# Optimization experiments

Measured on AMD Instinct MI355X. Metric: run time of the kernel, lower is better.

Reference implementation:

```python
import jax, jax.numpy as jnp
import numpy as np

PAD, BOS = 0, 1
EPS = 1e-08


def _lstm_cell(xt, h, c, wih, whh, bih, bhh):
    z = xt @ wih.T + h @ whh.T + bih + bhh
    i, f, g, o = jnp.split(z, 4, axis=-1)  # torch gate order i,f,g,o
    c = jax.nn.sigmoid(f) * c + jax.nn.sigmoid(i) * jnp.tanh(g)
    h = jax.nn.sigmoid(o) * jnp.tanh(c)
    return h, c


def _run_lstm(emb, wih, whh, bih, bhh):
    B, H = emb.shape[0], whh.shape[1]
    def step(carry, xt):
        h, c = _lstm_cell(xt, carry[0], carry[1], wih, whh, bih, bhh)
        return (h, c), h
    init = (jnp.zeros((B, H), emb.dtype), jnp.zeros((B, H), emb.dtype))
    (hT, cT), outs = jax.lax.scan(step, init, jnp.swapaxes(emb, 0, 1))
    return jnp.swapaxes(outs, 0, 1), hT, cT


def setup_inputs() -> dict:
    key = jax.random.key(0)
    V, H, B, S, T = 32000, 256, 8, 200, 51
    ks = jax.random.split(key, 24)
    def n(i, shape, s=0.02):
        return jax.random.normal(ks[i], shape, jnp.float32) * s
    x = jax.random.randint(ks[0], (B, S), 1, V)
    x = x.at[:, -1].set(V - 1)  # pins extended vocab size to 2V
    labels = jax.random.randint(ks[1], (B, T), 1, V)
    return {
        "x": x, "labels": labels, "ext_vocab_size": 2 * V,
        "emb_enc": n(2, (V, H)).at[PAD].set(0.0),
        "wih_f": n(3, (4 * H, H)), "whh_f": n(4, (4 * H, H)),
        "bih_f": jnp.zeros((4 * H,), jnp.float32), "bhh_f": jnp.zeros((4 * H,), jnp.float32),
        "wih_b": n(5, (4 * H, H)), "whh_b": n(6, (4 * H, H)),
        "bih_b": jnp.zeros((4 * H,), jnp.float32), "bhh_b": jnp.zeros((4 * H,), jnp.float32),
        "w_sel1": n(7, (H, 2 * H)), "b_sel1": jnp.zeros((H,), jnp.float32),
        "w_sel2": n(8, (1, H)), "b_sel2": jnp.zeros((1,), jnp.float32),
        "w_rh": n(9, (H, 2 * H)), "b_rh": jnp.zeros((H,), jnp.float32),
        "w_rc": n(10, (H, 2 * H)), "b_rc": jnp.zeros((H,), jnp.float32),
        "emb_dec": n(11, (V, H)).at[PAD].set(0.0),
        "wih_d": n(12, (4 * H, 3 * H)), "whh_d": n(13, (4 * H, H)),
        "bih_d": jnp.zeros((4 * H,), jnp.float32), "bhh_d": jnp.zeros((4 * H,), jnp.float32),
        "w_attn": n(14, (H, 4 * H)), "b_attn": jnp.zeros((H,), jnp.float32),
        "w_attn_v": n(15, (1, H)),
        "w_ptr": n(16, (1, 3 * H)), "b_ptr": jnp.zeros((1,), jnp.float32),
        "w_gen": n(17, (V, H)), "b_gen": jnp.zeros((V,), jnp.float32),
        "w_cov": n(18, (H, 1)), "b_cov": jnp.zeros((H,), jnp.float32),
    }


def reference(x, labels, ext_vocab_size, emb_enc, wih_f, whh_f, bih_f, bhh_f,
              wih_b, whh_b, bih_b, bhh_b, w_sel1, b_sel1, w_sel2, b_sel2,
              w_rh, b_rh, w_rc, b_rc, emb_dec, wih_d, whh_d, bih_d, bhh_d,
              w_attn, b_attn, w_attn_v, w_ptr, b_ptr, w_gen, b_gen, w_cov, b_cov):
    B, S = x.shape
    V, H = w_gen.shape
    # ---- Encoder: BiLSTM (no padding -> packing is identity; eval -> no dropout)
    emb = emb_enc[x]  # [B,S,H]
    out_f, h_f, c_f = _run_lstm(emb, wih_f, whh_f, bih_f, bhh_f)
    out_b_r, h_b, c_b = _run_lstm(emb[:, ::-1], wih_b, whh_b, bih_b, bhh_b)
    enc_out = jnp.concatenate([out_f, out_b_r[:, ::-1]], axis=-1)  # [B,S,2H]
    copy_probs = jax.nn.sigmoid(
        (jnp.tanh(enc_out @ w_sel1.T + b_sel1) @ w_sel2.T + b_sel2)[..., 0])  # [B,S]
    # ---- bidirectional state reduction
    h0 = jax.nn.relu(jnp.concatenate([h_f, h_b], -1) @ w_rh.T + b_rh)
    c0 = jax.nn.relu(jnp.concatenate([c_f, c_b], -1) @ w_rc.T + b_rc)
    # ---- Decoder loop (teacher forcing): inputs = [BOS, labels[:,1:T-1]]
    dec_in = jnp.concatenate(
        [jnp.full((B, 1), BOS, labels.dtype), labels[:, 1:-1]], axis=1)  # [B,T-1]
    mask_cp = (copy_probs > EPS).astype(jnp.float32)
    rows = jnp.arange(B)[:, None]

    def step(carry, tok):
        h, c, cov = carry
        cov_feat = cov[..., None] * w_cov[:, 0] + b_cov  # [B,S,H]
        feats = jnp.concatenate(
            [enc_out, jnp.broadcast_to(h[:, None, :], (B, S, H)), cov_feat], axis=-1)
        e = jnp.tanh(feats @ w_attn.T + b_attn)           # [B,S,H]
        attn = jax.nn.softmax(e @ w_attn_v[0], axis=1)    # [B,S]
        attn = attn * mask_cp
        attn = attn / (attn.sum(1, keepdims=True) + 1e-10)
        cov = cov + attn
        ctx = jnp.einsum('bs,bsd->bd', attn, enc_out)     # [B,2H]
        h, c = _lstm_cell(jnp.concatenate([emb_dec[tok], ctx], -1), h, c,
                          wih_d, whh_d, bih_d, bhh_d)
        p_gen = jax.nn.sigmoid(jnp.concatenate([ctx, h], -1) @ w_ptr.T + b_ptr)  # [B,1]
        vocab_dist = jax.nn.softmax(h @ w_gen.T + b_gen, axis=-1)  # [B,V]
        dist = jnp.zeros((B, ext_vocab_size), jnp.float32)
        dist = dist.at[:, :V].set(p_gen * vocab_dist)
        dist = dist.at[rows, x].add((1.0 - p_gen) * attn)  # pointer/copy scatter-add
        return (h, c, cov), dist

    cov0 = jnp.zeros((B, S), jnp.float32)
    _, outs = jax.lax.scan(step, (h0, c0, cov0), dec_in.T)
    outputs = jnp.swapaxes(outs, 0, 1)  # [B,T-1,EV]
    # ---- loss (faithful: CE treats the mixture distribution as logits)
    targets = labels[:, 1:]
    logp = jax.nn.log_softmax(outputs, axis=-1)
    nll = -jnp.take_along_axis(logp, targets[..., None], axis=-1)[..., 0]
    valid = (targets != PAD).astype(jnp.float32)
    loss_ce = (nll * valid).sum() / valid.sum()
    m = (x != PAD).astype(jnp.float32)
    lp = jnp.clip(jnp.log(copy_probs), -100.0, None)
    l1p = jnp.clip(jnp.log1p(-copy_probs), -100.0, None)
    bce = -(m * lp + (1.0 - m) * l1p)
    loss = loss_ce + 1.0 * (bce * m).sum() / m.sum()
    return outputs, loss
```

## Files before the change

### kernel.cpp

```cpp
#include <hip/hip_runtime.h>
#include <hip/hip_bf16.h>
#include <stdint.h>


#define DEVI __device__ __forceinline__
#define AT_RLX __ATOMIC_RELAXED
#define SC_AGT __HIP_MEMORY_SCOPE_AGENT

static constexpr size_t OFF_ACC   = 0;
static constexpr size_t OFF_FLAGE = 4;
static constexpr size_t OFF_FLAGD = 36;
static constexpr size_t ZERO_FLOATS = 200;
static constexpr size_t OFF_CTX   = 256;
static constexpr size_t OFF_EMB   = 4352;
static constexpr size_t OFF_HSEL  = OFF_EMB;
static constexpr size_t OFF_HP    = OFF_EMB;
static constexpr size_t OFF_DHP   = OFF_EMB;
static constexpr size_t OFF_DPE   = OFF_EMB + 8192;
static constexpr size_t OFF_DCX   = OFF_EMB + 20992;
static constexpr size_t DTAG_FLOATS = 53760;
static constexpr size_t OFF_PREF  = OFF_EMB  + 409600;
static constexpr size_t OFF_PREB  = OFF_PREF + 1638400;
static constexpr size_t OFF_BIAS  = OFF_PREB + 1638400;
static constexpr size_t OFF_HB    = OFF_BIAS + 3072;
static constexpr size_t OFF_HFIN  = OFF_HB   + 8192;
static constexpr size_t OFF_CFIN  = OFF_HFIN + 4096;
static constexpr size_t OFF_ENCOUT= OFF_CFIN + 4096;
static constexpr size_t OFF_MASK  = OFF_ENCOUT + 819200;
static constexpr size_t OFF_C0    = OFF_MASK + 1600;
static constexpr size_t OFF_EP    = OFF_C0   + 2048;
static constexpr size_t OFF_WCP   = OFF_EP   + 409600;
static constexpr size_t OFF_BCP   = OFF_WCP  + 256;
static constexpr size_t OFF_DEMB  = OFF_BCP  + 256;
static constexpr size_t OFF_DPRE  = OFF_DEMB + 102400;
static constexpr size_t OFF_HBUF  = OFF_DPRE + 409600;
static constexpr size_t OFF_CS    = OFF_HBUF + 4096;
static constexpr size_t OFF_HS    = OFF_CS   + 204800;
static constexpr size_t OFF_AS    = OFF_HS   + 102400;
static constexpr size_t OFF_PG    = OFF_AS   + 80000;
static constexpr size_t OFF_PE    = OFF_PG   + 512;

DEVI float sigf(float x)      { return 1.0f / (1.0f + __expf(-x)); }
DEVI float tanh_fast(float x) { return 1.0f - 2.0f / (1.0f + __expf(2.0f * x)); }
DEVI float ald(const float* p)  { return __hip_atomic_load((float*)p, AT_RLX, SC_AGT); }
DEVI void  ast(float* p, float v){ __hip_atomic_store(p, v, AT_RLX, SC_AGT); }
DEVI unsigned long long aldu(const unsigned long long* p) {
  return __hip_atomic_load((unsigned long long*)p, AT_RLX, SC_AGT);
}
DEVI void astu(unsigned long long* p, unsigned long long v) {
  __hip_atomic_store(p, v, AT_RLX, SC_AGT);
}

__global__ __launch_bounds__(256) void k_biassum(
    const float* bih_f, const float* bhh_f, const float* bih_b, const float* bhh_b,
    const float* bih_d, const float* bhh_d, float* ws) {
  int i = blockIdx.x * 256 + threadIdx.x;
  int which = i >> 10, jj = i & 1023;
  float v = (which == 0) ? bih_f[jj] + bhh_f[jj]
          : (which == 1) ? bih_b[jj] + bhh_b[jj]
                         : bih_d[jj] + bhh_d[jj];
  ws[OFF_BIAS + i] = v;
}

__global__ __launch_bounds__(256) void k_embed(
    const int* xin, const int* labels, const float* emb_enc, const float* emb_dec, float* ws) {
  int r = blockIdx.x, h = threadIdx.x;
  if (r < 1600) {
    int t = r >> 3, b = r & 7;
    ws[OFF_EMB + (size_t)r * 256 + h] = emb_enc[(size_t)xin[b * 200 + t] * 256 + h];
  } else {
    int r2 = r - 1600;
    int t = r2 >> 3, b = r2 & 7;
    int tok = (t == 0) ? 1 : labels[b * 51 + t];
    ws[OFF_DEMB + (size_t)r2 * 256 + h] = emb_dec[(size_t)tok * 256 + h];
  }
}

template<int BM, int BN, int TM, int TN, int CMAP, int ACT, int AMAP>
__global__ __launch_bounds__(256) void k_gemm(
    const float* __restrict__ A, const float* __restrict__ B,
    const float* __restrict__ bias, float* __restrict__ C,
    int M, int K, int ldb, int ldc) {
  __shared__ float As[16][BM];
  __shared__ float Bs[16][BN];
  const int tid = threadIdx.x;
  const int tx = tid & 15, ty = tid >> 4;
  const int m0 = blockIdx.x * BM, n0 = blockIdx.y * BN;
  float acc[TM][TN];
#pragma unroll
  for (int i = 0; i < TM; ++i)
#pragma unroll
    for (int q = 0; q < TN; ++q) acc[i][q] = 0.f;

  for (int kk = 0; kk < K; kk += 16) {
#pragma unroll
    for (int e = tid; e < BM * 4; e += 256) {
      int m = e >> 2, k4 = (e & 3) * 4;
      int gm0 = m0 + m;
      float4 v = {0.f, 0.f, 0.f, 0.f};
      if (gm0 < M) {
        int gm = AMAP ? (((199 - (gm0 >> 3)) << 3) + (gm0 & 7)) : gm0;
        v = *(const float4*)(A + (size_t)gm * K + kk + k4);
      }
      As[k4 + 0][m] = v.x; As[k4 + 1][m] = v.y; As[k4 + 2][m] = v.z; As[k4 + 3][m] = v.w;
    }
#pragma unroll
    for (int e = tid; e < BN * 4; e += 256) {
      int n = e >> 2, k4 = (e & 3) * 4;
      float4 v = *(const float4*)(B + (size_t)(n0 + n) * ldb + kk + k4);
      Bs[k4 + 0][n] = v.x; Bs[k4 + 1][n] = v.y; Bs[k4 + 2][n] = v.z; Bs[k4 + 3][n] = v.w;
    }
    __syncthreads();
#pragma unroll
    for (int k = 0; k < 16; ++k) {
      float a[TM], bv[TN];
#pragma unroll
      for (int i = 0; i < TM; ++i) a[i] = As[k][ty * TM + i];
#pragma unroll
      for (int q = 0; q < TN; ++q) bv[q] = Bs[k][tx * TN + q];
#pragma unroll
      for (int i = 0; i < TM; ++i)
#pragma unroll
        for (int q = 0; q < TN; ++q) acc[i][q] += a[i] * bv[q];
    }
    __syncthreads();
  }
#pragma unroll
  for (int i = 0; i < TM; ++i) {
    int gm = m0 + ty * TM + i;
    if (gm >= M) continue;
    size_t base;
    if (CMAP == 1) { int t = gm >> 3, b = gm & 7; base = (size_t)(b * 50 + t) * 64000; }
    else            base = (size_t)gm * ldc;
#pragma unroll
    for (int q = 0; q < TN; ++q) {
      int n = n0 + tx * TN + q;
      float v = acc[i][q] + bias[n];
      if (ACT == 1) v = tanh_fast(v);
      C[base + n] = v;
    }
  }
}

__global__ __launch_bounds__(512, 1) void k_encoder(
    const float* __restrict__ whh_f, const float* __restrict__ whh_b, float* __restrict__ ws) {
  __shared__ float hs2[2048];
  __shared__ float zs[512];
  const int dir = blockIdx.x >> 4;
  const int p   = blockIdx.x & 15;
  const int u0  = p * 16;
  const float* whh = dir ? whh_b : whh_f;
  const float* pre = ws + (dir ? OFF_PREB : OFF_PREF);
  unsigned long long* hp = (unsigned long long*)(ws + OFF_HP);
  const int tid = threadIdx.x;
  const int kc4 = tid & 15;
  const int jp  = tid >> 4;
  const int jj0 = jp * 2, jj1 = jj0 + 1;
  const int jg0 = (jj0 >> 4) * 256 + u0 + (jj0 & 15);
  const int jg1 = (jj1 >> 4) * 256 + u0 + (jj1 & 15);
  float4 W0[4], W1[4];
  {
    const float* w0 = whh + (size_t)jg0 * 256 + kc4 * 16;
    const float* w1 = whh + (size_t)jg1 * 256 + kc4 * 16;
#pragma unroll
    for (int q = 0; q < 4; ++q) { W0[q] = *(const float4*)(w0 + q * 4);
                                  W1[q] = *(const float4*)(w1 + q * 4); }
  }
  const int jlf = kc4 >> 3, bf = kc4 & 7;
  const int jjf = jp * 2 + jlf;
  const int jf  = (jjf >> 4) * 256 + u0 + (jjf & 15);
  const int zsl = (jjf >> 4) * 128 + (jjf & 15) * 8 + bf;
  const int wb_ = tid >> 6;
  const int kk0 = (tid * 4) & 255;
  const int wdst = wb_ * 256 + ((kk0 >> 2) & 3) * 64 + (kk0 >> 4) * 4;
  const int ui2 = tid & 15, b2 = tid >> 4;
  float c_reg = 0.f;
  float* enc = ws + OFF_ENCOUT;

  for (int t = 0; t < 200; ++t) {
    float pre_v = pre[((size_t)t * 8 + bf) * 1024 + jf];
    float acc[16];
#pragma unroll
    for (int i = 0; i < 16; ++i) acc[i] = 0.f;
    if (t > 0) {
      unsigned long long* src = hp + (size_t)((((t + 1) & 1) * 2 + dir) * 2048) + tid * 4;
      const unsigned long long e = (unsigned long long)(unsigned)t;
      unsigned long long a0, a1, a2, a3;
      for (;;) {
        a0 = aldu(src + 0); a1 = aldu(src + 1); a2 = aldu(src + 2); a3 = aldu(src + 3);
        if (((a0 >> 32) == e) && ((a1 >> 32) == e) &&
            ((a2 >> 32) == e) && ((a3 >> 32) == e)) break;
        __builtin_amdgcn_s_sleep(1);
      }
      float4 hv;
      hv.x = __uint_as_float((unsigned)a0);
      hv.y = __uint_as_float((unsigned)a1);
      hv.z = __uint_as_float((unsigned)a2);
      hv.w = __uint_as_float((unsigned)a3);
      *(float4*)(&hs2[wdst]) = hv;
    }
    __syncthreads();
    if (t > 0) {
#pragma unroll
      for (int b = 0; b < 8; ++b) {
        const float* hb = &hs2[b * 256 + kc4 * 4];
#pragma unroll
        for (int q = 0; q < 4; ++q) {
          float4 h4 = *(const float4*)(hb + q * 64);
          acc[b]     = fmaf(W0[q].x, h4.x, acc[b]);
          acc[b]     = fmaf(W0[q].y, h4.y, acc[b]);
          acc[b]     = fmaf(W0[q].z, h4.z, acc[b]);
          acc[b]     = fmaf(W0[q].w, h4.w, acc[b]);
          acc[8 + b] = fmaf(W1[q].x, h4.x, acc[8 + b]);
          acc[8 + b] = fmaf(W1[q].y, h4.y, acc[8 + b]);
          acc[8 + b] = fmaf(W1[q].z, h4.z, acc[8 + b]);
          acc[8 + b] = fmaf(W1[q].w, h4.w, acc[8 + b]);
        }
      }
    }
    {
      bool h8 = (kc4 & 8) != 0;
#pragma unroll
      for (int i = 0; i < 8; ++i) {
        float send = h8 ? acc[i] : acc[i + 8];
        float keep = h8 ? acc[i + 8] : acc[i];
        acc[i] = keep + __shfl_xor(send, 8);
      }
      bool h4b = (kc4 & 4) != 0;
#pragma unroll
      for (int i = 0; i < 4; ++i) {
        float send = h4b ? acc[i] : acc[i + 4];
        float keep = h4b ? acc[i + 4] : acc[i];
        acc[i] = keep + __shfl_xor(send, 4);
      }
      bool h2b = (kc4 & 2) != 0;
#pragma unroll
      for (int i = 0; i < 2; ++i) {
        float send = h2b ? acc[i] : acc[i + 2];
        float keep = h2b ? acc[i + 2] : acc[i];
        acc[i] = keep + __shfl_xor(send, 2);
      }
      bool h1b = (kc4 & 1) != 0;
      {
        float send = h1b ? acc[0] : acc[1];
        float keep = h1b ? acc[1] : acc[0];
        acc[0] = keep + __shfl_xor(send, 1);
      }
    }
    zs[zsl] = acc[0] + pre_v;
    __syncthreads();
    if (tid < 128) {
      int i0 = ui2 * 8 + b2;
      float zi = zs[i0], zf = zs[128 + i0], zg = zs[256 + i0], zo = zs[384 + i0];
      float cn = sigf(zf) * c_reg + sigf(zi) * tanh_fast(zg);
      float hn = sigf(zo) * tanh_fast(cn);
      c_reg = cn;
      int uu = u0 + ui2;
      if (t < 199) {
        unsigned long long pk =
            ((unsigned long long)(unsigned)(t + 1) << 32) |
            (unsigned long long)__float_as_uint(hn);
        astu(hp + (size_t)(((t & 1) * 2 + dir) * 2048) + b2 * 256 + uu, pk);
      }
      int s = dir ? (199 - t) : t;
      enc[((size_t)b2 * 200 + s) * 512 + dir * 256 + uu] = hn;
      if (t == 199) {
        ws[OFF_HFIN + (size_t)(dir * 8 + b2) * 256 + uu] = hn;
        ws[OFF_CFIN + (size_t)(dir * 8 + b2) * 256 + uu] = cn;
      }
    }
  }
}

__global__ __launch_bounds__(64) void k_selbce(
    const float* w_sel2, const float* b_sel2, const int* xin, float* ws) {
  int r = blockIdx.x, lane = threadIdx.x;
  float pacc = 0.f;
#pragma unroll
  for (int i = 0; i < 4; ++i) {
    int k = lane + 64 * i;
    pacc += ws[OFF_HSEL + (size_t)r * 256 + k] * w_sel2[k];
  }
#pragma unroll
  for (int m = 1; m < 64; m <<= 1) pacc += __shfl_xor(pacc, m);
  if (lane == 0) {
    float cp = sigf(pacc + b_sel2[0]);
    ws[OFF_MASK + r] = (cp > 1e-8f) ? 1.f : 0.f;
    int b = r / 200, s = r % 200;
    float m = (xin[b * 200 + s] != 0) ? 1.f : 0.f;
    if (m > 0.f) {
      float lp = fmaxf(logf(cp), -100.f);
      atomicAdd(ws + OFF_ACC + 2, -lp);
    }
    atomicAdd(ws + OFF_ACC + 3, m);
  }
}

__global__ __launch_bounds__(256) void k_wcp(
    const float* w_attn, const float* w_cov, const float* b_cov, float* ws) {
  int jj = threadIdx.x;
  float a = 0.f, c = 0.f;
  for (int h = 0; h < 256; ++h) {
    float w = w_attn[(size_t)jj * 1024 + 768 + h];
    a += w * w_cov[h];
    c += w * b_cov[h];
  }
  ws[OFF_WCP + jj] = a;
  ws[OFF_BCP + jj] = c;
}

__global__ __launch_bounds__(256) void k_h0c0(
    const float* w_rh, const float* b_rh, const float* w_rc, const float* b_rc, float* ws) {
  int b = blockIdx.x, jj = threadIdx.x;
  const float* hf  = ws + OFF_HFIN + (size_t)b * 256;
  const float* hbk = ws + OFF_HFIN + 2048 + (size_t)b * 256;
  const float* cf  = ws + OFF_CFIN + (size_t)b * 256;
  const float* cbk = ws + OFF_CFIN + 2048 + (size_t)b * 256;
  float ah = b_rh[jj], ac = b_rc[jj];
  for (int k = 0; k < 256; ++k) {
    ah += hf[k] * w_rh[(size_t)jj * 512 + k];
    ac += cf[k] * w_rc[(size_t)jj * 512 + k];
  }
  for (int k = 0; k < 256; ++k) {
    ah += hbk[k] * w_rh[(size_t)jj * 512 + 256 + k];
    ac += cbk[k] * w_rc[(size_t)jj * 512 + 256 + k];
  }
  ws[OFF_C0 + (size_t)b * 256 + jj] = fmaxf(ac, 0.f);
  unsigned long long* hp2 = (unsigned long long*)(ws + OFF_DHP);
  hp2[(size_t)b * 256 + jj] = (unsigned long long)__float_as_uint(fmaxf(ah, 0.f));
}

__global__ __launch_bounds__(512, 1) void k_decoder(
    const float* __restrict__ wih_d, const float* __restrict__ whh_d,
    const float* __restrict__ w_attn, const float* __restrict__ w_attn_v,
    float* __restrict__ ws) {
  __shared__ float hc_s[8 * 768];
  __shared__ float h_pad[264];
  __shared__ float hw_q[64];
  __shared__ float e_s[256];
  __shared__ float at_s[256], cv_s[256], msk_s[256];
  __shared__ float zs_l[256];
  __shared__ float wcq_s[64], bcq_s[64], wvq_s[64];
  __shared__ float mS_s[2];
  const int g = blockIdx.x, tid = threadIdx.x;
  const int b1 = g >> 2, sq = g & 3, s0 = sq * 50;
  unsigned long long* hp2 = (unsigned long long*)(ws + OFF_DHP);
  unsigned long long* pe2 = (unsigned long long*)(ws + OFF_DPE);
  unsigned long long* cx2 = (unsigned long long*)(ws + OFF_DCX);
  const int jl = tid >> 3, kq = tid & 7;
  const int kseg = tid & 15, row_l = tid >> 4;
  const int u_l = row_l & 7, gate = row_l >> 3;
  const int j = gate * 256 + g * 8 + u_l;
  float4 W48[12];
#pragma unroll
  for (int q = 0; q < 12; ++q) {
    int k0 = 4 * kseg + 64 * q;
    W48[q] = (k0 < 512) ? *(const float4*)(wih_d + (size_t)j * 768 + 256 + k0)
                        : *(const float4*)(whh_d + (size_t)j * 256 + (k0 - 512));
  }
  float4 W32[8];
  {
    const float* wsrc = w_attn + (size_t)(sq * 64 + jl) * 1024 + 512 + kq * 32;
#pragma unroll
    for (int q = 0; q < 8; ++q) W32[q] = *(const float4*)(wsrc + q * 4);
  }
  const int u_c = tid & 7, b_c = tid >> 3;
  float c_reg = (tid < 64) ? ws[OFF_C0 + (size_t)b_c * 256 + g * 8 + u_c] : 0.f;
  for (int s = tid; s < 256; s += 512) {
    msk_s[s] = (s < 200) ? ws[OFF_MASK + b1 * 200 + s] : 0.f;
    cv_s[s] = 0.f;
  }
  if (tid < 64) {
    wcq_s[tid] = ws[OFF_WCP + sq * 64 + tid];
    bcq_s[tid] = ws[OFF_BCP + sq * 64 + tid];
    wvq_s[tid] = w_attn_v[sq * 64 + tid];
  }
  __syncthreads();

  for (int t = 0; t < 50; ++t) {
    const int rb = t & 1, wb = 1 - rb;
    const unsigned long long tgH = (unsigned long long)(unsigned)t;
    const unsigned long long tgP = (unsigned long long)(unsigned)(t + 1);
    if (tid < 256) {
      unsigned long long* src = hp2 + (size_t)rb * 2048 + b1 * 256 + tid;
      unsigned long long v;
      for (;;) {
        v = aldu(src);
        if ((v >> 32) == tgH) break;
        __builtin_amdgcn_s_sleep(1);
      }
      h_pad[(tid >> 5) * 33 + (tid & 31)] = __uint_as_float((unsigned)v);
    }
    __syncthreads();
    {
      float a = 0.f;
      const float* hq = &h_pad[kq * 33];
#pragma unroll
      for (int q = 0; q < 8; ++q) {
        float4 h4 = { hq[q * 4 + 0], hq[q * 4 + 1], hq[q * 4 + 2], hq[q * 4 + 3] };
        a = fmaf(W32[q].x, h4.x, a);
        a = fmaf(W32[q].y, h4.y, a);
        a = fmaf(W32[q].z, h4.z, a);
        a = fmaf(W32[q].w, h4.w, a);
      }
      a += __shfl_xor(a, 1);
      a += __shfl_xor(a, 2);
      a += __shfl_xor(a, 4);
      if (kq == 0) hw_q[jl] = a;
    }
    __syncthreads();
    if (tid < 200) {
      const int s = tid;
      float cv = cv_s[s];
      const float* ep = ws + OFF_EP + ((size_t)(b1 * 200 + s)) * 256 + sq * 64;
      float pe = 0.f;
#pragma unroll
      for (int i4 = 0; i4 < 16; ++i4) {
        float4 e4 = *(const float4*)(ep + i4 * 4);
        float4 h4 = *(const float4*)(&hw_q[i4 * 4]);
        float4 w4 = *(const float4*)(&wcq_s[i4 * 4]);
        float4 b4 = *(const float4*)(&bcq_s[i4 * 4]);
        float4 v4 = *(const float4*)(&wvq_s[i4 * 4]);
        pe = fmaf(tanh_fast(e4.x + h4.x + cv * w4.x + b4.x), v4.x, pe);
        pe = fmaf(tanh_fast(e4.y + h4.y + cv * w4.y + b4.y), v4.y, pe);
        pe = fmaf(tanh_fast(e4.z + h4.z + cv * w4.z + b4.z), v4.z, pe);
        pe = fmaf(tanh_fast(e4.w + h4.w + cv * w4.w + b4.w), v4.w, pe);
      }
      astu(pe2 + (size_t)(sq * 8 + b1) * 200 + s,
           (tgP << 32) | (unsigned long long)__float_as_uint(pe));
    }

    if (tid < 200) {
      float esum = 0.f;
#pragma unroll
      for (int q = 0; q < 4; ++q) {
        unsigned long long* src = pe2 + (size_t)(q * 8 + b1) * 200 + tid;
        unsigned long long v;
        for (;;) {
          v = aldu(src);
          if ((v >> 32) == tgP) break;
          __builtin_amdgcn_s_sleep(1);
        }
        esum += __uint_as_float((unsigned)v);
      }
      e_s[tid] = esum;
    }
    __syncthreads();
    if (tid < 64) {
      float m = -1e30f;
#pragma unroll
      for (int i = 0; i < 4; ++i) {
        int s = tid + 64 * i;
        if (s < 200) m = fmaxf(m, e_s[s]);
      }
#pragma unroll
      for (int md = 1; md < 64; md <<= 1) m = fmaxf(m, __shfl_xor(m, md));
      float es = 0.f, ems = 0.f;
#pragma unroll
      for (int i = 0; i < 4; ++i) {
        int s = tid + 64 * i;
        if (s < 200) {
          float e = __expf(e_s[s] - m);
          es += e; ems += e * msk_s[s];
        }
      }
#pragma unroll
      for (int md = 1; md < 64; md <<= 1) { es += __shfl_xor(es, md); ems += __shfl_xor(ems, md); }
      if (tid == 0) { mS_s[0] = m; mS_s[1] = 1.0f / (ems + 1e-10f * es); }
    }
    __syncthreads();
    if (tid < 200) {
      float a = __expf(e_s[tid] - mS_s[0]) * msk_s[tid] * mS_s[1];
      at_s[tid] = a;
      cv_s[tid] += a;
      if (tid >= s0 && tid < s0 + 50)
        ws[OFF_AS + ((size_t)t * 8 + b1) * 200 + tid] = a;
    }
    __syncthreads();
    {
      float ca = 0.f;
      const float* ebase = ws + OFF_ENCOUT + ((size_t)(b1 * 200 + s0)) * 512 + tid;
#pragma unroll 10
      for (int s2 = 0; s2 < 50; ++s2)
        ca = fmaf(at_s[s0 + s2], ebase[(size_t)s2 * 512], ca);
      astu(cx2 + (size_t)(sq * 8 + b1) * 512 + tid,
           (tgP << 32) | (unsigned long long)__float_as_uint(ca));
    }

    for (int e = tid; e < 6144; e += 512) {
      int bb = e / 768, kk2 = e % 768;
      float val;
      if (kk2 < 512) {
        unsigned long long* p0 = cx2 + (size_t)(0 * 8 + bb) * 512 + kk2;
        unsigned long long* p1 = cx2 + (size_t)(1 * 8 + bb) * 512 + kk2;
        unsigned long long* p2 = cx2 + (size_t)(2 * 8 + bb) * 512 + kk2;
        unsigned long long* p3 = cx2 + (size_t)(3 * 8 + bb) * 512 + kk2;
        unsigned long long v0, v1, v2, v3;
        for (;;) {
          v0 = aldu(p0); v1 = aldu(p1); v2 = aldu(p2); v3 = aldu(p3);
          if (((v0 >> 32) == tgP) && ((v1 >> 32) == tgP) &&
              ((v2 >> 32) == tgP) && ((v3 >> 32) == tgP)) break;
          __builtin_amdgcn_s_sleep(1);
        }
        val = (__uint_as_float((unsigned)v0) + __uint_as_float((unsigned)v1)) +
              (__uint_as_float((unsigned)v2) + __uint_as_float((unsigned)v3));
      } else {
        unsigned long long* src = hp2 + (size_t)rb * 2048 + bb * 256 + (kk2 - 512);
        unsigned long long v;
        for (;;) {
          v = aldu(src);
          if ((v >> 32) == tgH) break;
          __builtin_amdgcn_s_sleep(1);
        }
        val = __uint_as_float((unsigned)v);
      }
      hc_s[e] = val;
    }
    __syncthreads();
    if (g < 8) ws[OFF_CS + ((size_t)t * 8 + g) * 512 + tid] = hc_s[g * 768 + tid];
    float acc[8];
#pragma unroll
    for (int b = 0; b < 8; ++b) acc[b] = 0.f;
#pragma unroll
    for (int q = 0; q < 12; ++q) {
      int k0 = 4 * kseg + 64 * q;
#pragma unroll
      for (int b = 0; b < 8; ++b) {
        float4 h4 = *(const float4*)(&hc_s[b * 768 + k0]);
        acc[b] = fmaf(W48[q].x, h4.x, acc[b]);
        acc[b] = fmaf(W48[q].y, h4.y, acc[b]);
        acc[b] = fmaf(W48[q].z, h4.z, acc[b]);
        acc[b] = fmaf(W48[q].w, h4.w, acc[b]);
      }
    }
    {
      bool h8 = (kseg & 8) != 0;
#pragma unroll
      for (int i = 0; i < 4; ++i) {
        float send = h8 ? acc[i] : acc[i + 4];
        float keep = h8 ? acc[i + 4] : acc[i];
        acc[i] = keep + __shfl_xor(send, 8);
      }
      bool h4b = (kseg & 4) != 0;
#pragma unroll
      for (int i = 0; i < 2; ++i) {
        float send = h4b ? acc[i] : acc[i + 2];
        float keep = h4b ? acc[i + 2] : acc[i];
        acc[i] = keep + __shfl_xor(send, 4);
      }
      bool h2b = (kseg & 2) != 0;
      {
        float send = h2b ? acc[0] : acc[1];
        float keep = h2b ? acc[1] : acc[0];
        acc[0] = keep + __shfl_xor(send, 2);
      }
      acc[0] += __shfl_xor(acc[0], 1);
    }
    {
      int bz = kseg >> 1;
      float z = acc[0] + ws[OFF_DPRE + ((size_t)t * 8 + bz) * 1024 + j];
      if ((kseg & 1) == 0) zs_l[row_l * 8 + bz] = z;
    }
    __syncthreads();
    if (tid < 64) {
      float zi = zs_l[(0  + u_c) * 8 + b_c];
      float zf = zs_l[(8  + u_c) * 8 + b_c];
      float zg = zs_l[(16 + u_c) * 8 + b_c];
      float zo = zs_l[(24 + u_c) * 8 + b_c];
      float cn = sigf(zf) * c_reg + sigf(zi) * tanh_fast(zg);
      float hn = sigf(zo) * tanh_fast(cn);
      c_reg = cn;
      astu(hp2 + (size_t)wb * 2048 + b_c * 256 + g * 8 + u_c,
           (tgP << 32) | (unsigned long long)__float_as_uint(hn));
      ws[OFF_HS + ((size_t)t * 8 + b_c) * 256 + g * 8 + u_c] = hn;
    }
  }
}

__global__ __launch_bounds__(64) void k_pgen(const float* w_ptr, const float* b_ptr, float* ws) {
  int r = blockIdx.x, lane = threadIdx.x;
  float p = 0.f;
#pragma unroll
  for (int i = 0; i < 12; ++i) {
    int k = lane + 64 * i;
    float v = (k < 512) ? ws[OFF_CS + (size_t)r * 512 + k]
                        : ws[OFF_HS + (size_t)r * 256 + (k - 512)];
    p += v * w_ptr[k];
  }
#pragma unroll
  for (int m = 1; m < 64; m <<= 1) p += __shfl_xor(p, m);
  if (lane == 0) ws[OFF_PG + r] = sigf(p + b_ptr[0]);
}

__global__ __launch_bounds__(256) void k_v2(const int* xin, const int* labels, float* ws, float* out) {
  __shared__ float redm[256], reds[256];
  __shared__ int xv[200];
  __shared__ float s1sh, corrsh;
  int r = blockIdx.x, tid = threadIdx.x;
  int tt = r >> 3, b = r & 7;
  float* row = out + (size_t)(b * 50 + tt) * 64000;
  for (int i = tid; i < 200; i += 256) xv[i] = xin[b * 200 + i];
  float m = -1e30f, s = 0.f;
  for (int i = tid; i < 32000; i += 256) {
    float z = row[i];
    float nm = fmaxf(m, z);
    s = s * __expf(m - nm) + __expf(z - nm);
    m = nm;
  }
  redm[tid] = m; reds[tid] = s;
  __syncthreads();
  for (int st = 128; st >= 1; st >>= 1) {
    if (tid < st) {
      float m2 = redm[tid + st], s2 = reds[tid + st];
      float M = fmaxf(redm[tid], m2);
      reds[tid] = reds[tid] * __expf(redm[tid] - M) + s2 * __expf(m2 - M);
      redm[tid] = M;
    }
    __syncthreads();
  }
  float mx = redm[0], sum = reds[0];
  float pg = ws[OFF_PG + r];
  __syncthreads();
  float s1 = 0.f;
  float inv = 1.0f / sum;
  for (int i = tid; i < 32000; i += 256) {
    float z = row[i];
    float d = pg * (__expf(z - mx) * inv);
    row[i] = d;
    s1 += __expf(d);
  }
  for (int i = 32000 + tid; i < 64000; i += 256) row[i] = 0.0f;
  reds[tid] = s1;
  __syncthreads();
  for (int st = 128; st >= 1; st >>= 1) { if (tid < st) reds[tid] += reds[tid + st]; __syncthreads(); }
  if (tid == 0) { s1sh = reds[0]; corrsh = 0.f; }
  __syncthreads();
  if (tid < 200) {
    int v = xv[tid];
    bool own = true;
    for (int s2 = 0; s2 < tid; ++s2) if (xv[s2] == v) { own = false; break; }
    if (own) {
      float delta = 0.f;
      for (int s2 = tid; s2 < 200; ++s2)
        if (xv[s2] == v) delta += ws[OFF_AS + (size_t)r * 200 + s2];
      delta *= (1.0f - pg);
      float base = row[v];
      row[v] = base + delta;
      atomicAdd(&corrsh, __expf(base + delta) - __expf(base));
    }
  }
  __syncthreads();
  if (tid == 0) {
    float lse = logf(s1sh + corrsh + 32000.0f);
    int tgt = labels[b * 51 + tt + 1];
    float dt = row[tgt];
    float valid = (tgt != 0) ? 1.f : 0.f;
    atomicAdd(ws + OFF_ACC + 0, valid * (lse - dt));
    atomicAdd(ws + OFF_ACC + 1, valid);
  }
}

__global__ void k_loss(float* ws, float* out, int out_size) {
  out[out_size - 1] = ws[OFF_ACC + 0] / ws[OFF_ACC + 1] + ws[OFF_ACC + 2] / ws[OFF_ACC + 3];
}

extern "C" void kernel_launch(void* const* d_in, const int* in_sizes, int n_in,
                              void* d_out, int out_size, void* d_ws, size_t ws_size,
                              hipStream_t stream) {
  (void)in_sizes; (void)n_in; (void)ws_size;
  const int*   x       = (const int*)  d_in[0];
  const int*   labels  = (const int*)  d_in[1];
  const float* emb_enc = (const float*)d_in[3];
  const float* wih_f   = (const float*)d_in[4];
  const float* whh_f   = (const float*)d_in[5];
  const float* bih_f   = (const float*)d_in[6];
  const float* bhh_f   = (const float*)d_in[7];
  const float* wih_b   = (const float*)d_in[8];
  const float* whh_b   = (const float*)d_in[9];
  const float* bih_b   = (const float*)d_in[10];
  const float* bhh_b   = (const float*)d_in[11];
  const float* w_sel1  = (const float*)d_in[12];
  const float* b_sel1  = (const float*)d_in[13];
  const float* w_sel2  = (const float*)d_in[14];
  const float* b_sel2  = (const float*)d_in[15];
  const float* w_rh    = (const float*)d_in[16];
  const float* b_rh    = (const float*)d_in[17];
  const float* w_rc    = (const float*)d_in[18];
  const float* b_rc    = (const float*)d_in[19];
  const float* emb_dec = (const float*)d_in[20];
  const float* wih_d   = (const float*)d_in[21];
  const float* whh_d   = (const float*)d_in[22];
  const float* bih_d   = (const float*)d_in[23];
  const float* bhh_d   = (const float*)d_in[24];
  const float* w_attn  = (const float*)d_in[25];
  const float* b_attn  = (const float*)d_in[26];
  const float* w_attn_v= (const float*)d_in[27];
  const float* w_ptr   = (const float*)d_in[28];
  const float* b_ptr   = (const float*)d_in[29];
  const float* w_gen   = (const float*)d_in[30];
  const float* b_gen   = (const float*)d_in[31];
  const float* w_cov   = (const float*)d_in[32];
  const float* b_cov   = (const float*)d_in[33];
  float* ws  = (float*)d_ws;
  float* out = (float*)d_out;

  hipMemsetAsync(d_ws, 0, ZERO_FLOATS * 4, stream);
  k_biassum<<<12, 256, 0, stream>>>(bih_f, bhh_f, bih_b, bhh_b, bih_d, bhh_d, ws);
  k_embed<<<2000, 256, 0, stream>>>(x, labels, emb_enc, emb_dec, ws);
  k_gemm<64,64,4,4,0,0,0><<<dim3(25,16), 256, 0, stream>>>(ws+OFF_EMB,  wih_f, ws+OFF_BIAS,      ws+OFF_PREF, 1600, 256, 256, 1024);
  k_gemm<64,64,4,4,0,0,1><<<dim3(25,16), 256, 0, stream>>>(ws+OFF_EMB,  wih_b, ws+OFF_BIAS+1024, ws+OFF_PREB, 1600, 256, 256, 1024);
  k_gemm<64,64,4,4,0,0,0><<<dim3(7,16),  256, 0, stream>>>(ws+OFF_DEMB, wih_d, ws+OFF_BIAS+2048, ws+OFF_DPRE, 400,  256, 768, 1024);
  hipMemsetAsync((void*)(ws + OFF_HP), 0, (size_t)2 * 2 * 2048 * sizeof(unsigned long long), stream);
  k_encoder<<<32, 512, 0, stream>>>(whh_f, whh_b, ws);
  k_gemm<64,64,4,4,0,1,0><<<dim3(25,4),  256, 0, stream>>>(ws+OFF_ENCOUT, w_sel1, b_sel1, ws+OFF_HSEL, 1600, 512, 512, 256);
  k_selbce<<<1600, 64, 0, stream>>>(w_sel2, b_sel2, x, ws);
  hipMemsetAsync((void*)(ws + OFF_EMB), 0, DTAG_FLOATS * sizeof(float), stream);
  k_gemm<64,64,4,4,0,0,0><<<dim3(25,4),  256, 0, stream>>>(ws+OFF_ENCOUT, w_attn, b_attn, ws+OFF_EP, 1600, 512, 1024, 256);
  k_wcp<<<1, 256, 0, stream>>>(w_attn, w_cov, b_cov, ws);
  k_h0c0<<<8, 256, 0, stream>>>(w_rh, b_rh, w_rc, b_rc, ws);
  k_decoder<<<32, 512, 0, stream>>>(wih_d, whh_d, w_attn, w_attn_v, ws);
  k_pgen<<<400, 64, 0, stream>>>(w_ptr, b_ptr, ws);
  k_gemm<128,128,8,8,1,0,0><<<dim3(4,250), 256, 0, stream>>>(ws+OFF_HS, w_gen, b_gen, out, 400, 256, 256, 64000);
  k_v2<<<400, 256, 0, stream>>>(x, labels, ws, out);
  k_loss<<<1, 1, 0, stream>>>(ws, out, out_size);
}
```

Measured before the change: 2.140 ms.

## Compute full attention energies per block, dropping cross-block energy exchange

Each decoder block now computes the full 256-wide attention projection and all 200 energies for its batch row itself, rather than a quarter slice followed by a global tagged exchange of partial energies among four blocks. The context vector partition also changes: each block reduces all 200 positions for a 128-column slice, combining the four partial sums in shared memory, so consumers poll one tagged value instead of four. This removes one global spin-wait round per timestep at the cost of four times the redundant attention arithmetic per block and many more registers held for weights (128 floats per thread).

```diff
diff --git a/kernel.cpp b/kernel.cpp
--- a/kernel.cpp
+++ b/kernel.cpp
@@ -16,9 +16,8 @@
 static constexpr size_t OFF_HSEL  = OFF_EMB;
 static constexpr size_t OFF_HP    = OFF_EMB;
 static constexpr size_t OFF_DHP   = OFF_EMB;
-static constexpr size_t OFF_DPE   = OFF_EMB + 8192;
-static constexpr size_t OFF_DCX   = OFF_EMB + 20992;
-static constexpr size_t DTAG_FLOATS = 53760;
+static constexpr size_t OFF_DCX   = OFF_EMB + 8192;
+static constexpr size_t DTAG_FLOATS = 16384;
 static constexpr size_t OFF_PREF  = OFF_EMB  + 409600;
 static constexpr size_t OFF_PREB  = OFF_PREF + 1638400;
 static constexpr size_t OFF_BIAS  = OFF_PREB + 1638400;
@@ -336,18 +335,22 @@
     float* __restrict__ ws) {
   __shared__ float hc_s[8 * 768];
   __shared__ float h_pad[264];
-  __shared__ float hw_q[64];
-  __shared__ float e_s[256];
-  __shared__ float at_s[256], cv_s[256], msk_s[256];
+  __shared__ float hw_s[256];
+  __shared__ float e_s[200];
+  __shared__ float at_s[200], cv_s[200], msk_s[200];
   __shared__ float zs_l[256];
-  __shared__ float wcq_s[64], bcq_s[64], wvq_s[64];
+  __shared__ float wc_s[256], bc_s[256], wv_s[256];
   __shared__ float mS_s[2];
+  __shared__ float cxp_s[4][128];
   const int g = blockIdx.x, tid = threadIdx.x;
   const int b1 = g >> 2, sq = g & 3, s0 = sq * 50;
   unsigned long long* hp2 = (unsigned long long*)(ws + OFF_DHP);
-  unsigned long long* pe2 = (unsigned long long*)(ws + OFF_DPE);
   unsigned long long* cx2 = (unsigned long long*)(ws + OFF_DCX);
-  const int jl = tid >> 3, kq = tid & 7;
+  const int jW = tid >> 1, khW = tid & 1;
+  float4 W32[32];
+#pragma unroll
+  for (int q = 0; q < 32; ++q)
+    W32[q] = *(const float4*)(w_attn + (size_t)jW * 1024 + 512 + khW * 128 + q * 4);
   const int kseg = tid & 15, row_l = tid >> 4;
   const int u_l = row_l & 7, gate = row_l >> 3;
   const int j = gate * 256 + g * 8 + u_l;
@@ -358,22 +361,18 @@
     W48[q] = (k0 < 512) ? *(const float4*)(wih_d + (size_t)j * 768 + 256 + k0)
                         : *(const float4*)(whh_d + (size_t)j * 256 + (k0 - 512));
   }
-  float4 W32[8];
-  {
-    const float* wsrc = w_attn + (size_t)(sq * 64 + jl) * 1024 + 512 + kq * 32;
-#pragma unroll
-    for (int q = 0; q < 8; ++q) W32[q] = *(const float4*)(wsrc + q * 4);
-  }
+  const int sE = tid >> 1, hE = tid & 1;
+  const int cC = tid & 127, qC = tid >> 7;
   const int u_c = tid & 7, b_c = tid >> 3;
   float c_reg = (tid < 64) ? ws[OFF_C0 + (size_t)b_c * 256 + g * 8 + u_c] : 0.f;
-  for (int s = tid; s < 256; s += 512) {
-    msk_s[s] = (s < 200) ? ws[OFF_MASK + b1 * 200 + s] : 0.f;
-    cv_s[s] = 0.f;
-  }
-  if (tid < 64) {
-    wcq_s[tid] = ws[OFF_WCP + sq * 64 + tid];
-    bcq_s[tid] = ws[OFF_BCP + sq * 64 + tid];
-    wvq_s[tid] = w_attn_v[sq * 64 + tid];
+  if (tid < 200) {
+    msk_s[tid] = ws[OFF_MASK + b1 * 200 + tid];
+    cv_s[tid] = 0.f;
+  }
+  if (tid < 256) {
+    wc_s[tid] = ws[OFF_WCP + tid];
+    bc_s[tid] = ws[OFF_BCP + tid];
+    wv_s[tid] = w_attn_v[tid];
   }
   __syncthreads();
 
@@ -394,116 +393,101 @@
     __syncthreads();
     {
       float a = 0.f;
-      const float* hq = &h_pad[kq * 33];
-#pragma unroll
-      for (int q = 0; q < 8; ++q) {
-        float4 h4 = { hq[q * 4 + 0], hq[q * 4 + 1], hq[q * 4 + 2], hq[q * 4 + 3] };
-        a = fmaf(W32[q].x, h4.x, a);
-        a = fmaf(W32[q].y, h4.y, a);
-        a = fmaf(W32[q].z, h4.z, a);
-        a = fmaf(W32[q].w, h4.w, a);
+#pragma unroll
+      for (int q = 0; q < 32; ++q) {
+        int k = khW * 128 + q * 4;
+        const float* hq = &h_pad[(k >> 5) * 33 + (k & 31)];
+        float4 w4 = W32[q];
+        a = fmaf(w4.x, hq[0], a);
+        a = fmaf(w4.y, hq[1], a);
+        a = fmaf(w4.z, hq[2], a);
+        a = fmaf(w4.w, hq[3], a);
       }
       a += __shfl_xor(a, 1);
-      a += __shfl_xor(a, 2);
-      a += __shfl_xor(a, 4);
-      if (kq == 0) hw_q[jl] = a;
-    }
-    __syncthreads();
-    if (tid < 200) {
-      const int s = tid;
-      float cv = cv_s[s];
-      const float* ep = ws + OFF_EP + ((size_t)(b1 * 200 + s)) * 256 + sq * 64;
+      if (khW == 0) hw_s[jW] = a;
+    }
+    __syncthreads();
+    if (sE < 200) {
+      float cv = cv_s[sE];
+      const float* ep  = ws + OFF_EP + ((size_t)(b1 * 200 + sE)) * 256 + hE * 128;
+      const float* hwp = &hw_s[hE * 128];
+      const float* wcp = &wc_s[hE * 128];
+      const float* bcp = &bc_s[hE * 128];
+      const float* wvp = &wv_s[hE * 128];
       float pe = 0.f;
 #pragma unroll
-      for (int i4 = 0; i4 < 16; ++i4) {
+      for (int i4 = 0; i4 < 32; ++i4) {
         float4 e4 = *(const float4*)(ep + i4 * 4);
-        float4 h4 = *(const float4*)(&hw_q[i4 * 4]);
-        float4 w4 = *(const float4*)(&wcq_s[i4 * 4]);
-        float4 b4 = *(const float4*)(&bcq_s[i4 * 4]);
-        float4 v4 = *(const float4*)(&wvq_s[i4 * 4]);
+        float4 h4 = *(const float4*)(hwp + i4 * 4);
+        float4 w4 = *(const float4*)(wcp + i4 * 4);
+        float4 b4 = *(const float4*)(bcp + i4 * 4);
+        float4 v4 = *(const float4*)(wvp + i4 * 4);
         pe = fmaf(tanh_fast(e4.x + h4.x + cv * w4.x + b4.x), v4.x, pe);
         pe = fmaf(tanh_fast(e4.y + h4.y + cv * w4.y + b4.y), v4.y, pe);
         pe = fmaf(tanh_fast(e4.z + h4.z + cv * w4.z + b4.z), v4.z, pe);
         pe = fmaf(tanh_fast(e4.w + h4.w + cv * w4.w + b4.w), v4.w, pe);
       }
-      astu(pe2 + (size_t)(sq * 8 + b1) * 200 + s,
-           (tgP << 32) | (unsigned long long)__float_as_uint(pe));
-    }
-
+      pe += __shfl_xor(pe, 1);
+      if (hE == 0) e_s[sE] = pe;
+    }
+    __syncthreads();
+    if (tid < 64) {
+      float m = -1e30f;
+#pragma unroll
+      for (int i = 0; i < 4; ++i) {
+        int s = tid + 64 * i;
+        if (s < 200) m = fmaxf(m, e_s[s]);
+      }
+#pragma unroll
+      for (int md = 1; md < 64; md <<= 1) m = fmaxf(m, __shfl_xor(m, md));
+      float es = 0.f, ems = 0.f;
+#pragma unroll
+      for (int i = 0; i < 4; ++i) {
+        int s = tid + 64 * i;
+        if (s < 200) {
+          float e = __expf(e_s[s] - m);
+          es += e; ems += e * msk_s[s];
+        }
+      }
+#pragma unroll
+      for (int md = 1; md < 64; md <<= 1) { es += __shfl_xor(es, md); ems += __shfl_xor(ems, md); }
+      if (tid == 0) { mS_s[0] = m; mS_s[1] = 1.0f / (ems + 1e-10f * es); }
+    }
+    __syncthreads();
     if (tid < 200) {
-      float esum = 0.f;
-#pragma unroll
-      for (int q = 0; q < 4; ++q) {
-        unsigned long long* src = pe2 + (size_t)(q * 8 + b1) * 200 + tid;
+      float a = __expf(e_s[tid] - mS_s[0]) * msk_s[tid] * mS_s[1];
+      at_s[tid] = a;
+      cv_s[tid] += a;
+      if (tid >= s0 && tid < s0 + 50)
+        ws[OFF_AS + ((size_t)t * 8 + b1) * 200 + tid] = a;
+    }
+    __syncthreads();
+    {
+      float ca = 0.f;
+      const float* ebase = ws + OFF_ENCOUT + ((size_t)(b1 * 200 + qC * 50)) * 512 + sq * 128 + cC;
+#pragma unroll 10
+      for (int s2 = 0; s2 < 50; ++s2)
+        ca = fmaf(at_s[qC * 50 + s2], ebase[(size_t)s2 * 512], ca);
+      cxp_s[qC][cC] = ca;
+    }
+    __syncthreads();
+    if (tid < 128) {
+      float ca = (cxp_s[0][tid] + cxp_s[1][tid]) + (cxp_s[2][tid] + cxp_s[3][tid]);
+      astu(cx2 + (size_t)b1 * 512 + sq * 128 + tid,
+           (tgP << 32) | (unsigned long long)__float_as_uint(ca));
+    }
+    for (int e = tid; e < 6144; e += 512) {
+      int bb = e / 768, kk2 = e % 768;
+      float val;
+      if (kk2 < 512) {
+        unsigned long long* src = cx2 + (size_t)bb * 512 + kk2;
         unsigned long long v;
         for (;;) {
           v = aldu(src);
           if ((v >> 32) == tgP) break;
           __builtin_amdgcn_s_sleep(1);
         }
-        esum += __uint_as_float((unsigned)v);
-      }
-      e_s[tid] = esum;
-    }
-    __syncthreads();
-    if (tid < 64) {
-      float m = -1e30f;
-#pragma unroll
-      for (int i = 0; i < 4; ++i) {
-        int s = tid + 64 * i;
-        if (s < 200) m = fmaxf(m, e_s[s]);
-      }
-#pragma unroll
-      for (int md = 1; md < 64; md <<= 1) m = fmaxf(m, __shfl_xor(m, md));
-      float es = 0.f, ems = 0.f;
-#pragma unroll
-      for (int i = 0; i < 4; ++i) {
-        int s = tid + 64 * i;
-        if (s < 200) {
-          float e = __expf(e_s[s] - m);
-          es += e; ems += e * msk_s[s];
-        }
-      }
-#pragma unroll
-      for (int md = 1; md < 64; md <<= 1) { es += __shfl_xor(es, md); ems += __shfl_xor(ems, md); }
-      if (tid == 0) { mS_s[0] = m; mS_s[1] = 1.0f / (ems + 1e-10f * es); }
-    }
-    __syncthreads();
-    if (tid < 200) {
-      float a = __expf(e_s[tid] - mS_s[0]) * msk_s[tid] * mS_s[1];
-      at_s[tid] = a;
-      cv_s[tid] += a;
-      if (tid >= s0 && tid < s0 + 50)
-        ws[OFF_AS + ((size_t)t * 8 + b1) * 200 + tid] = a;
-    }
-    __syncthreads();
-    {
-      float ca = 0.f;
-      const float* ebase = ws + OFF_ENCOUT + ((size_t)(b1 * 200 + s0)) * 512 + tid;
-#pragma unroll 10
-      for (int s2 = 0; s2 < 50; ++s2)
-        ca = fmaf(at_s[s0 + s2], ebase[(size_t)s2 * 512], ca);
-      astu(cx2 + (size_t)(sq * 8 + b1) * 512 + tid,
-           (tgP << 32) | (unsigned long long)__float_as_uint(ca));
-    }
-
-    for (int e = tid; e < 6144; e += 512) {
-      int bb = e / 768, kk2 = e % 768;
-      float val;
-      if (kk2 < 512) {
-        unsigned long long* p0 = cx2 + (size_t)(0 * 8 + bb) * 512 + kk2;
-        unsigned long long* p1 = cx2 + (size_t)(1 * 8 + bb) * 512 + kk2;
-        unsigned long long* p2 = cx2 + (size_t)(2 * 8 + bb) * 512 + kk2;
-        unsigned long long* p3 = cx2 + (size_t)(3 * 8 + bb) * 512 + kk2;
-        unsigned long long v0, v1, v2, v3;
-        for (;;) {
-          v0 = aldu(p0); v1 = aldu(p1); v2 = aldu(p2); v3 = aldu(p3);
-          if (((v0 >> 32) == tgP) && ((v1 >> 32) == tgP) &&
-              ((v2 >> 32) == tgP) && ((v3 >> 32) == tgP)) break;
-          __builtin_amdgcn_s_sleep(1);
-        }
-        val = (__uint_as_float((unsigned)v0) + __uint_as_float((unsigned)v1)) +
-              (__uint_as_float((unsigned)v2) + __uint_as_float((unsigned)v3));
+        val = __uint_as_float((unsigned)v);
       } else {
         unsigned long long* src = hp2 + (size_t)rb * 2048 + bb * 256 + (kk2 - 512);
         unsigned long long v;
```

New measurement: 2.505 ms. 17.0% more time.
